# Kernel optimization log

Hardware: AMD Instinct MI355X
Metric: run time of the kernel (lower is better)

The kernel has to match this reference:

```python
import jax, jax.numpy as jnp
import numpy as np

B, S, D, H, DH, L, W, V, FF, HID = 2, 4096, 768, 12, 64, 12, 256, 50265, 3072, 384
SEL = np.arange(64) * 64  # index_select positions


def layer_norm(x, g, b):
    m = x.mean(-1, keepdims=True)
    v = ((x - m) ** 2).mean(-1, keepdims=True)
    return (x - m) * jax.lax.rsqrt(v + 1e-5) * g + b


def band_attention(q, k, v, key_mask):
    # q,k,v: [B,H,S,DH]; key_mask: [B,S] bool. Sliding window attention,
    # one-sided window W (total window 2W+1), via overlapping key chunks.
    nc = S // W
    qc = q.reshape(B, H, nc, W, DH)
    kp = jnp.pad(k, ((0, 0), (0, 0), (W, W), (0, 0)))
    vp = jnp.pad(v, ((0, 0), (0, 0), (W, W), (0, 0)))
    idx = jnp.arange(nc)[:, None] * W + jnp.arange(3 * W)[None, :]  # [nc,3W]
    kc = kp[:, :, idx]  # [B,H,nc,3W,DH]
    vc = vp[:, :, idx]
    scores = jnp.einsum('bhcid,bhcjd->bhcij', qc, kc) / np.float32(np.sqrt(DH))
    i = jnp.arange(W)[:, None]
    j = jnp.arange(3 * W)[None, :]
    band = (j >= i) & (j <= i + 2 * W)  # |key_pos - query_pos| <= W
    kmp = jnp.pad(key_mask, ((0, 0), (W, W)))
    kmc = kmp[:, idx]  # [B,nc,3W] key validity (in-range and non-pad)
    m = band[None, None, None] & kmc[:, None, :, None, :]
    scores = jnp.where(m, scores, -1e9)
    p = jax.nn.softmax(scores, axis=-1)
    ctx = jnp.einsum('bhcij,bhcjd->bhcid', p, vc)
    return ctx.reshape(B, H, S, DH)


def split_heads(x):
    return x.reshape(B, S, H, DH).transpose(0, 2, 1, 3)


def encoder(h, key_mask, layers):
    def step(h, p):
        Wq, bq, Wk, bk, Wv, bv, Wo, bo, g1, be1, W1, bf1, W2, bf2, g2, be2 = p
        q = split_heads(h @ Wq + bq)
        k = split_heads(h @ Wk + bk)
        v = split_heads(h @ Wv + bv)
        ctx = band_attention(q, k, v, key_mask).transpose(0, 2, 1, 3).reshape(B, S, D)
        h = layer_norm(h + ctx @ Wo + bo, g1, be1)
        ff = jax.nn.gelu(h @ W1 + bf1, approximate=False) @ W2 + bf2
        h = layer_norm(h + ff, g2, be2)
        return h, None
    h, _ = jax.lax.scan(jax.checkpoint(step), h, layers)
    return h


def lstm_scan(xs, Wi, Wh, b, reverse):
    # xs: [S,B,D]; torch gate order i,f,g,o
    def cell(carry, xt):
        h, c = carry
        g = xt @ Wi.T + h @ Wh.T + b
        gi, gf, gg, go = jnp.split(g, 4, axis=-1)
        c = jax.nn.sigmoid(gf) * c + jax.nn.sigmoid(gi) * jnp.tanh(gg)
        h = jax.nn.sigmoid(go) * jnp.tanh(c)
        return (h, c), h
    init = (jnp.zeros((B, HID), xs.dtype), jnp.zeros((B, HID), xs.dtype))
    _, hs = jax.lax.scan(cell, init, xs, reverse=reverse)
    return hs


def setup_inputs() -> dict:
    key = jax.random.key(0)
    ks = iter(jax.random.split(key, 40))
    std = 0.02
    n = lambda shape: jax.random.normal(next(ks), shape, jnp.float32) * std
    d = {
        'x': jax.random.randint(next(ks), (B, S), 0, V),
        'emb_w': n((V, D)), 'emb_p': n((S, D)),
        'ln_eg': jnp.ones((D,)), 'ln_eb': jnp.zeros((D,)),
        'Wq': n((L, D, D)), 'bq': jnp.zeros((L, D)),
        'Wk': n((L, D, D)), 'bk': jnp.zeros((L, D)),
        'Wv': n((L, D, D)), 'bv': jnp.zeros((L, D)),
        'Wo': n((L, D, D)), 'bo': jnp.zeros((L, D)),
        'ln1g': jnp.ones((L, D)), 'ln1b': jnp.zeros((L, D)),
        'W1': n((L, D, FF)), 'bf1': jnp.zeros((L, FF)),
        'W2': n((L, FF, D)), 'bf2': jnp.zeros((L, D)),
        'ln2g': jnp.ones((L, D)), 'ln2b': jnp.zeros((L, D)),
        'wi_f': n((4 * HID, D)), 'wh_f': n((4 * HID, HID)), 'b_f': jnp.zeros((4 * HID,)),
        'wi_b': n((4 * HID, D)), 'wh_b': n((4 * HID, HID)), 'b_b': jnp.zeros((4 * HID,)),
    }
    return d


def reference(x, emb_w, emb_p, ln_eg, ln_eb, Wq, bq, Wk, bk, Wv, bv, Wo, bo,
              ln1g, ln1b, W1, bf1, W2, bf2, ln2g, ln2b,
              wi_f, wh_f, b_f, wi_b, wh_b, b_b):
    key_mask = (x != 0)  # mask = (x != 0).float()
    h = layer_norm(emb_w[x] + emb_p[None, :S], ln_eg, ln_eb)
    layers = (Wq, bq, Wk, bk, Wv, bv, Wo, bo, ln1g, ln1b, W1, bf1, W2, bf2, ln2g, ln2b)
    h = encoder(h, key_mask, layers)
    xs = h.transpose(1, 0, 2)  # [S,B,D]
    hf = lstm_scan(xs, wi_f, wh_f, b_f, False)
    hb = lstm_scan(xs, wi_b, wh_b, b_b, True)
    rnn = jnp.concatenate([hf, hb], axis=-1).transpose(1, 0, 2)  # [B,S,D]
    return rnn[:, SEL]  # index_select -> [B,64,D]
```

## Files before the change

### kernel.cpp

```cpp
#include <hip/hip_runtime.h>


typedef short short8 __attribute__((ext_vector_type(8)));
typedef float float4_ __attribute__((ext_vector_type(4)));
typedef unsigned int uint2v __attribute__((ext_vector_type(2)));

#define GLOBAL_AS __attribute__((address_space(1)))
#define LDS_AS __attribute__((address_space(3)))

__device__ __forceinline__ short f2bf(float f) {
  union { float f; unsigned u; } x; x.f = f;
  unsigned r = (x.u + 0x7FFFu + ((x.u >> 16) & 1u)) >> 16;
  return (short)r;
}
__device__ __forceinline__ float sigm(float x) { return 1.0f / (1.0f + __expf(-x)); }
__device__ __forceinline__ float tanh_f(float x) { float e = __expf(2.0f * x); return 1.0f - 2.0f / (e + 1.0f); }

__device__ __forceinline__ void load_lds16(const void* g, void* l) {
  __builtin_amdgcn_global_load_lds((const GLOBAL_AS unsigned int*)g,
                                   (LDS_AS unsigned int*)l, 16, 0, 0);
}

__global__ void embed_kernel(const int* __restrict__ x, const float* __restrict__ emb_w,
                             const float* __restrict__ emb_p, float* __restrict__ tmp,
                             float* __restrict__ kmask) {
  int row = blockIdx.x;
  int s = row & 4095;
  int tok = x[row];
  const float* ew = emb_w + (size_t)tok * 768;
  const float* ep = emb_p + (size_t)s * 768;
  for (int i = threadIdx.x; i < 768; i += 256)
    tmp[(size_t)row * 768 + i] = ew[i] + ep[i];
  if (threadIdx.x == 0) kmask[row] = (tok != 0) ? 1.0f : 0.0f;
}

__global__ __launch_bounds__(256) void ln_kernel(const float* __restrict__ in,
    const float* __restrict__ g, const float* __restrict__ b,
    float* __restrict__ outf, short* __restrict__ outb, int rows) {
  int wave = threadIdx.x >> 6, lane = threadIdx.x & 63;
  int row = blockIdx.x * 4 + wave;
  if (row >= rows) return;
  const float* p = in + (size_t)row * 768;
  float v[12]; float s = 0.f, s2 = 0.f;
#pragma unroll
  for (int j = 0; j < 12; ++j) { v[j] = p[lane + j * 64]; s += v[j]; s2 += v[j] * v[j]; }
#pragma unroll
  for (int k = 1; k < 64; k <<= 1) { s += __shfl_xor(s, k); s2 += __shfl_xor(s2, k); }
  float mean = s * (1.0f / 768.0f);
  float var = s2 * (1.0f / 768.0f) - mean * mean;
  float rstd = rsqrtf(var + 1e-5f);
#pragma unroll
  for (int j = 0; j < 12; ++j) {
    int c = lane + j * 64;
    float o = (v[j] - mean) * rstd * g[c] + b[c];
    outf[(size_t)row * 768 + c] = o;
    outb[(size_t)row * 768 + c] = f2bf(o);
  }
}

__global__ __launch_bounds__(256) void prep_layer_kernel(
    const float* __restrict__ Wq, const float* __restrict__ Wk, const float* __restrict__ Wv,
    const float* __restrict__ Wo, const float* __restrict__ W1, const float* __restrict__ W2,
    const float* __restrict__ bq, const float* __restrict__ bk, const float* __restrict__ bv,
    short* __restrict__ wqkv, short* __restrict__ wo, short* __restrict__ w1,
    short* __restrict__ w2, float* __restrict__ biasqkv, int layer) {
  int bid = blockIdx.x;
  if (bid >= 6912) {
    int i = (bid - 6912) * 256 + threadIdx.x;
    if (i < 2304) {
      float v = (i < 768) ? bq[layer * 768 + i]
               : (i < 1536) ? bk[layer * 768 + i - 768] : bv[layer * 768 + i - 1536];
      biasqkv[i] = v;
    }
    return;
  }
  const float* src; short* dst; int R, C, tr, tc;
  if (bid < 1728) {
    int m = bid / 576; int tloc = bid % 576;
    src = (m == 0 ? Wq : (m == 1 ? Wk : Wv)) + (size_t)layer * 768 * 768;
    dst = wqkv + (size_t)m * 768 * 768; R = 768; C = 768; tr = tloc / 24; tc = tloc % 24;
  } else if (bid < 2304) {
    int tloc = bid - 1728; src = Wo + (size_t)layer * 768 * 768; dst = wo;
    R = 768; C = 768; tr = tloc / 24; tc = tloc % 24;
  } else if (bid < 4608) {
    int tloc = bid - 2304; src = W1 + (size_t)layer * 768 * 3072; dst = w1;
    R = 768; C = 3072; tr = tloc / 96; tc = tloc % 96;
  } else {
    int tloc = bid - 4608; src = W2 + (size_t)layer * 3072 * 768; dst = w2;
    R = 3072; C = 768; tr = tloc / 24; tc = tloc % 24;
  }
  __shared__ float tile[32][33];
  int tx = threadIdx.x & 31, ty = threadIdx.x >> 5;
#pragma unroll
  for (int i = 0; i < 4; ++i)
    tile[ty + i * 8][tx] = src[(size_t)(tr * 32 + ty + i * 8) * C + tc * 32 + tx];
  __syncthreads();
#pragma unroll
  for (int i = 0; i < 4; ++i) {
    int r = ty + i * 8;
    dst[(size_t)(tc * 32 + r) * R + tr * 32 + tx] = f2bf(tile[tx][r]);
  }
}

template <int MODE>
__global__ __launch_bounds__(256) void gemm_kernel(const short* __restrict__ A,
    const short* __restrict__ Bt, const float* __restrict__ bias,
    const float* __restrict__ res, float* __restrict__ outf, short* __restrict__ outb,
    int M, int N, int K, int ntn) {
  __shared__ short As[128 * 64];
  __shared__ short Bs[128 * 64];
  int tid = threadIdx.x;
  int wave = tid >> 6, lane = tid & 63;
  int l15 = lane & 15, qd = lane >> 4;
  int tm = blockIdx.x / ntn, tn = blockIdx.x % ntn;
  int wm = wave >> 1, wn = wave & 1;
  float4_ acc[4][4] = {};
  for (int k0 = 0; k0 < K; k0 += 64) {
    __syncthreads();
#pragma unroll
    for (int inst = 0; inst < 4; ++inst) {
      int i = inst * 256 + tid;
      const short* ga = A + (size_t)(tm * 128 + (i >> 3)) * K + k0 + (i & 7) * 8;
      const short* gb = Bt + (size_t)(tn * 128 + (i >> 3)) * K + k0 + (i & 7) * 8;
      int ldso = (inst * 256 + wave * 64) * 8;
      load_lds16(ga, &As[ldso]);
      load_lds16(gb, &Bs[ldso]);
    }
    __syncthreads();
#pragma unroll
    for (int ks = 0; ks < 2; ++ks) {
      short8 af[4], bf[4];
#pragma unroll
      for (int mt = 0; mt < 4; ++mt)
        af[mt] = *(const short8*)&As[(wm * 64 + mt * 16 + l15) * 64 + ks * 32 + qd * 8];
#pragma unroll
      for (int nt = 0; nt < 4; ++nt)
        bf[nt] = *(const short8*)&Bs[(wn * 64 + nt * 16 + l15) * 64 + ks * 32 + qd * 8];
#pragma unroll
      for (int mt = 0; mt < 4; ++mt)
#pragma unroll
        for (int nt = 0; nt < 4; ++nt)
          acc[mt][nt] = __builtin_amdgcn_mfma_f32_16x16x32_bf16(af[mt], bf[nt], acc[mt][nt], 0, 0, 0);
    }
  }
  int r0 = tm * 128 + wm * 64, c0 = tn * 128 + wn * 64;
#pragma unroll
  for (int nt = 0; nt < 4; ++nt) {
    int col = c0 + nt * 16 + l15;
    float bv = bias[col];
#pragma unroll
    for (int mt = 0; mt < 4; ++mt) {
      int rowb = r0 + mt * 16 + qd * 4;
#pragma unroll
      for (int r = 0; r < 4; ++r) {
        int row = rowb + r;
        float v = acc[mt][nt][r] + bv;
        if constexpr (MODE == 1) v = v * 0.5f * (1.0f + erff(v * 0.70710678f));
        if constexpr (MODE == 2) v += res[(size_t)row * N + col];
        if constexpr (MODE == 0 || MODE == 1) outb[(size_t)row * N + col] = f2bf(v);
        else outf[(size_t)row * N + col] = v;
      }
    }
  }
}

__global__ __launch_bounds__(256) void attn_kernel(const short* __restrict__ qkv,
    const float* __restrict__ kmask, short* __restrict__ ctx) {
  __shared__ short Ks[256 * 72];
  __shared__ short Vt[64 * 264];
  __shared__ float Ms[256];
  int bid = blockIdx.x;
  int qs = bid & 3; int c = (bid >> 2) & 15; int hh = bid >> 6;
  int head = hh % 12; int bt = hh / 12;
  int tid = threadIdx.x;
  int wave = tid >> 6, lane = tid & 63;
  int l15 = lane & 15, qd = lane >> 4;
  const float SCALE = 0.18033688f;

  short8 qf[2];
  {
    size_t srow = ((size_t)bt * 4096 + c * 256 + qs * 64 + wave * 16 + l15) * 2304;
#pragma unroll
    for (int ks = 0; ks < 2; ++ks)
      qf[ks] = *(const short8*)&qkv[srow + head * 64 + ks * 32 + qd * 8];
  }
  int iq = qs * 64 + wave * 16 + l15;

  float m_run = -1e9f, l_run = 0.0f;
  float4_ o4[4] = {};

  for (int kci = 0; kci < 3; ++kci) {
    int kc = c + kci - 1;
    if (kc < 0 || kc > 15) continue;
    __syncthreads();
    {
      int p = tid;
      size_t kr = ((size_t)bt * 4096 + kc * 256 + p) * 2304;
      int colv = (p & ~31) + (((p >> 2) & 3) << 3) + (((p >> 4) & 1) << 2) + (p & 3);
#pragma unroll
      for (int j8 = 0; j8 < 8; ++j8) {
        short8 kk = *(const short8*)&qkv[kr + 768 + head * 64 + j8 * 8];
        *(short8*)&Ks[p * 72 + j8 * 8] = kk;
        short8 vv = *(const short8*)&qkv[kr + 1536 + head * 64 + j8 * 8];
#pragma unroll
        for (int j = 0; j < 8; ++j) Vt[(j8 * 8 + j) * 264 + colv] = vv[j];
      }
      Ms[p] = kmask[bt * 4096 + kc * 256 + p];
    }
    __syncthreads();

    float4_ sc[16];
#pragma unroll
    for (int T = 0; T < 16; ++T) {
      float4_ a = {0.f, 0.f, 0.f, 0.f};
#pragma unroll
      for (int ks = 0; ks < 2; ++ks) {
        short8 kf = *(const short8*)&Ks[(T * 16 + l15) * 72 + ks * 32 + qd * 8];
        a = __builtin_amdgcn_mfma_f32_16x16x32_bf16(kf, qf[ks], a, 0, 0, 0);
      }
      sc[T] = a;
    }
    float cm = -1e9f;
#pragma unroll
    for (int T = 0; T < 16; ++T) {
      float4_ mk = *(const float4_*)&Ms[T * 16 + qd * 4];
#pragma unroll
      for (int r = 0; r < 4; ++r) {
        int key = T * 16 + qd * 4 + r;
        bool band = (kci == 1) || (kci == 0 ? (key >= iq) : (key <= iq));
        bool val = band && (mk[r] != 0.0f);
        float sv = val ? sc[T][r] * SCALE : -1e9f;
        sc[T][r] = sv;
        cm = fmaxf(cm, sv);
      }
    }
    cm = fmaxf(cm, __shfl_xor(cm, 16));
    cm = fmaxf(cm, __shfl_xor(cm, 32));
    float mnew = fmaxf(m_run, cm);
    float alpha = exp2f(m_run - mnew);
    m_run = mnew;
    l_run *= alpha;
#pragma unroll
    for (int mt = 0; mt < 4; ++mt) o4[mt] *= alpha;
#pragma unroll
    for (int T = 0; T < 16; ++T)
#pragma unroll
      for (int r = 0; r < 4; ++r) {
        float p = exp2f(sc[T][r] - mnew);
        sc[T][r] = p;
        l_run += p;
      }
#pragma unroll
    for (int ks = 0; ks < 8; ++ks) {
      short8 pb;
      pb[0] = f2bf(sc[2 * ks][0]);     pb[1] = f2bf(sc[2 * ks][1]);
      pb[2] = f2bf(sc[2 * ks][2]);     pb[3] = f2bf(sc[2 * ks][3]);
      pb[4] = f2bf(sc[2 * ks + 1][0]); pb[5] = f2bf(sc[2 * ks + 1][1]);
      pb[6] = f2bf(sc[2 * ks + 1][2]); pb[7] = f2bf(sc[2 * ks + 1][3]);
#pragma unroll
      for (int mt = 0; mt < 4; ++mt) {
        short8 va = *(const short8*)&Vt[(mt * 16 + l15) * 264 + ks * 32 + qd * 8];
        o4[mt] = __builtin_amdgcn_mfma_f32_16x16x32_bf16(va, pb, o4[mt], 0, 0, 0);
      }
    }
  }
  l_run += __shfl_xor(l_run, 16);
  l_run += __shfl_xor(l_run, 32);
  float rl = 1.0f / l_run;
  size_t crow = ((size_t)bt * 4096 + c * 256 + qs * 64 + wave * 16 + l15) * 768 + head * 64;
#pragma unroll
  for (int mt = 0; mt < 4; ++mt) {
    unsigned lo = (unsigned short)f2bf(o4[mt][0] * rl) |
                  ((unsigned)(unsigned short)f2bf(o4[mt][1] * rl) << 16);
    unsigned hi = (unsigned short)f2bf(o4[mt][2] * rl) |
                  ((unsigned)(unsigned short)f2bf(o4[mt][3] * rl) << 16);
    uint2v pk; pk[0] = lo; pk[1] = hi;
    *(uint2v*)&ctx[crow + mt * 16 + qd * 4] = pk;
  }
}

__global__ void lstm_prep_kernel(const float* __restrict__ wi_f, const float* __restrict__ wi_b,
    const float* __restrict__ wh_f, const float* __restrict__ wh_b,
    short* __restrict__ wi_bf, short* __restrict__ wh_bf) {
  size_t idx = (size_t)blockIdx.x * 256 + threadIdx.x;
  const size_t NWI = 1179648, NWH = 589824;
  if (idx < 2 * NWI) {
    const float* s = idx < NWI ? wi_f : wi_b;
    size_t k = idx < NWI ? idx : idx - NWI;
    wi_bf[idx] = f2bf(s[k]);
  } else {
    size_t k = idx - 2 * NWI;
    int d = k >= NWH;
    size_t kk = d ? k - NWH : k;
    int row = (int)(kk / 384), col = (int)(kk % 384);
    int w = row >> 7, g = (row >> 5) & 3, j = row & 31;
    const float* s = d ? wh_b : wh_f;
    wh_bf[k] = f2bf(s[(size_t)(g * 384 + w * 32 + j) * 384 + col]);
  }
}

__global__ void lstm_init_kernel(short* __restrict__ hbuf, unsigned* __restrict__ cnt) {
  int idx = blockIdx.x * 256 + threadIdx.x;
  if (idx < 24576) hbuf[idx] = 0;
  if (idx < 64) cnt[idx] = 0;
}

__global__ __launch_bounds__(256) void lstm_kernel(const short* __restrict__ Whb,
    const float* __restrict__ G, short* __restrict__ hbuf, unsigned* __restrict__ cnt,
    float* __restrict__ out) {
  int wg = blockIdx.x; int dir = wg / 12; int w = wg - dir * 12;
  int tid = threadIdx.x; int wave = tid >> 6; int lane = tid & 63;
  int l15 = lane & 15, qd = lane >> 4;
  __shared__ float gbuf[4][2][32];
  __shared__ float cst[64];
  short8 afrag[2][12];
#pragma unroll
  for (int tt = 0; tt < 2; ++tt)
#pragma unroll
    for (int ks = 0; ks < 12; ++ks)
      afrag[tt][ks] = *(const short8*)&Whb[((size_t)dir * 1536 + w * 128 + wave * 32 + tt * 16 + l15) * 384 + ks * 32 + qd * 8];
  if (tid < 64) cst[tid] = 0.0f;
  __syncthreads();
  unsigned* mycnt = cnt + dir * 16;
  for (int s = 0; s < 4096; ++s) {
    int t = dir ? (4095 - s) : s;
    if (s > 0) {
      if (tid == 0) {
        unsigned tgt = 12u * (unsigned)s;
        while (__hip_atomic_load(mycnt, __ATOMIC_ACQUIRE, __HIP_MEMORY_SCOPE_AGENT) < tgt)
          __builtin_amdgcn_s_sleep(1);
      }
      __syncthreads();
    }
    const short* hb = hbuf + (size_t)(dir * 2 + (s & 1)) * 16 * 384;
    short8 bfrag[12];
#pragma unroll
    for (int ks = 0; ks < 12; ++ks)
      bfrag[ks] = *(const short8*)&hb[l15 * 384 + ks * 32 + qd * 8];
    float gin[4] = {0.f, 0.f, 0.f, 0.f};
    if (tid < 64) {
      int j = tid & 31, bb = tid >> 5;
      const float* Gp = G + ((size_t)dir * 8192 + bb * 4096 + t) * 1536 + w * 32 + j;
#pragma unroll
      for (int g = 0; g < 4; ++g) gin[g] = Gp[g * 384];
    }
    float4_ acc0 = {0.f, 0.f, 0.f, 0.f}, acc1 = {0.f, 0.f, 0.f, 0.f};
#pragma unroll
    for (int ks = 0; ks < 12; ++ks) {
      acc0 = __builtin_amdgcn_mfma_f32_16x16x32_bf16(afrag[0][ks], bfrag[ks], acc0, 0, 0, 0);
      acc1 = __builtin_amdgcn_mfma_f32_16x16x32_bf16(afrag[1][ks], bfrag[ks], acc1, 0, 0, 0);
    }
    if (l15 < 2) {
#pragma unroll
      for (int r = 0; r < 4; ++r) {
        gbuf[wave][l15][qd * 4 + r] = acc0[r];
        gbuf[wave][l15][16 + qd * 4 + r] = acc1[r];
      }
    }
    __syncthreads();
    if (tid < 64) {
      int j = tid & 31, bb = tid >> 5;
      float gi = gbuf[0][bb][j] + gin[0];
      float gf = gbuf[1][bb][j] + gin[1];
      float gg = gbuf[2][bb][j] + gin[2];
      float go = gbuf[3][bb][j] + gin[3];
      float cc = sigm(gf) * cst[tid] + sigm(gi) * tanh_f(gg);
      cst[tid] = cc;
      float hh2 = sigm(go) * tanh_f(cc);
      hbuf[((size_t)(dir * 2 + ((s + 1) & 1)) * 16 + bb) * 384 + w * 32 + j] = f2bf(hh2);
      if ((t & 63) == 0)
        out[((size_t)bb * 64 + (t >> 6)) * 768 + dir * 384 + w * 32 + j] = hh2;
    }
    __threadfence();
    __syncthreads();
    if (tid == 0) atomicAdd(mycnt, 1u);
  }
}

extern "C" void kernel_launch(void* const* d_in, const int* in_sizes, int n_in,
                              void* d_out, int out_size, void* d_ws, size_t ws_size,
                              hipStream_t stream) {
  const int*   x     = (const int*)d_in[0];
  const float* emb_w = (const float*)d_in[1];
  const float* emb_p = (const float*)d_in[2];
  const float* ln_eg = (const float*)d_in[3];
  const float* ln_eb = (const float*)d_in[4];
  const float* Wq    = (const float*)d_in[5];
  const float* bq    = (const float*)d_in[6];
  const float* Wk    = (const float*)d_in[7];
  const float* bk    = (const float*)d_in[8];
  const float* Wv    = (const float*)d_in[9];
  const float* bv    = (const float*)d_in[10];
  const float* Wo    = (const float*)d_in[11];
  const float* bo    = (const float*)d_in[12];
  const float* ln1g  = (const float*)d_in[13];
  const float* ln1b  = (const float*)d_in[14];
  const float* W1    = (const float*)d_in[15];
  const float* bf1   = (const float*)d_in[16];
  const float* W2    = (const float*)d_in[17];
  const float* bf2   = (const float*)d_in[18];
  const float* ln2g  = (const float*)d_in[19];
  const float* ln2b  = (const float*)d_in[20];
  const float* wi_f  = (const float*)d_in[21];
  const float* wh_f  = (const float*)d_in[22];
  const float* b_f   = (const float*)d_in[23];
  const float* wi_b  = (const float*)d_in[24];
  const float* wh_b  = (const float*)d_in[25];
  const float* b_b   = (const float*)d_in[26];

  char* ws = (char*)d_ws;
  size_t off = 0;
  auto alloc = [&](size_t n) { size_t o = off; off += (n + 255) & ~(size_t)255; return o; };
  float* h_f32    = (float*)(ws + alloc(8192ull * 768 * 4));
  short* h_b16    = (short*)(ws + alloc(8192ull * 768 * 2));
  size_t alias0   = alloc(125829120ull);
  short* qkv      = (short*)(ws + alias0);
  short* ctx      = (short*)(ws + alias0 + 37748736ull);
  float* tmp      = (float*)(ws + alias0 + 50331648ull);
  short* ffn1     = (short*)(ws + alias0 + 75497472ull);
  float* G        = (float*)(ws + alias0);
  short* wqkv_t   = (short*)(ws + alloc(2304ull * 768 * 2));
  short* wo_t     = (short*)(ws + alloc(768ull * 768 * 2));
  short* w1_t     = (short*)(ws + alloc(3072ull * 768 * 2));
  short* w2_t     = (short*)(ws + alloc(768ull * 3072 * 2));
  float* biasqkv  = (float*)(ws + alloc(2304 * 4));
  short* wi_bf    = (short*)(ws + alloc(2ull * 1536 * 768 * 2));
  short* wh_bf    = (short*)(ws + alloc(2ull * 1536 * 384 * 2));
  short* hbuf     = (short*)(ws + alloc(2ull * 2 * 16 * 384 * 2));
  unsigned* cnt   = (unsigned*)(ws + alloc(256));
  float* kmask    = (float*)(ws + alloc(8192 * 4));
  if (ws_size < off) return;

  embed_kernel<<<8192, 256, 0, stream>>>(x, emb_w, emb_p, tmp, kmask);
  ln_kernel<<<2048, 256, 0, stream>>>(tmp, ln_eg, ln_eb, h_f32, h_b16, 8192);

  for (int l = 0; l < 12; ++l) {
    prep_layer_kernel<<<6921, 256, 0, stream>>>(Wq, Wk, Wv, Wo, W1, W2, bq, bk, bv,
                                                wqkv_t, wo_t, w1_t, w2_t, biasqkv, l);
    gemm_kernel<0><<<64 * 18, 256, 0, stream>>>(h_b16, wqkv_t, biasqkv, nullptr,
                                                nullptr, qkv, 8192, 2304, 768, 18);
    attn_kernel<<<1536, 256, 0, stream>>>(qkv, kmask, ctx);
    gemm_kernel<2><<<64 * 6, 256, 0, stream>>>(ctx, wo_t, bo + l * 768, h_f32,
                                               tmp, nullptr, 8192, 768, 768, 6);
    ln_kernel<<<2048, 256, 0, stream>>>(tmp, ln1g + l * 768, ln1b + l * 768, h_f32, h_b16, 8192);
    gemm_kernel<1><<<64 * 24, 256, 0, stream>>>(h_b16, w1_t, bf1 + l * 3072, nullptr,
                                                nullptr, ffn1, 8192, 3072, 768, 24);
    gemm_kernel<2><<<64 * 6, 256, 0, stream>>>(ffn1, w2_t, bf2 + l * 768, h_f32,
                                               tmp, nullptr, 8192, 768, 3072, 6);
    ln_kernel<<<2048, 256, 0, stream>>>(tmp, ln2g + l * 768, ln2b + l * 768, h_f32, h_b16, 8192);
  }

  lstm_prep_kernel<<<13824, 256, 0, stream>>>(wi_f, wi_b, wh_f, wh_b, wi_bf, wh_bf);
  gemm_kernel<3><<<64 * 12, 256, 0, stream>>>(h_b16, wi_bf, b_f, nullptr,
                                              G, nullptr, 8192, 1536, 768, 12);
  gemm_kernel<3><<<64 * 12, 256, 0, stream>>>(h_b16, wi_bf + 1536ull * 768, b_b, nullptr,
                                              G + 8192ull * 1536, nullptr, 8192, 1536, 768, 12);
  lstm_init_kernel<<<96, 256, 0, stream>>>(hbuf, cnt);
  lstm_kernel<<<24, 256, 0, stream>>>(wh_bf, G, hbuf, cnt, (float*)d_out);
}
```

Measured before the change: 23.43 ms.

## Restructure LSTM recurrence to 4 workgroups per direction with lighter cross-block sync

Each LSTM direction now runs on 4 workgroups instead of 12. Each workgroup keeps 96 hidden units of recurrent weights in registers (6 MFMA tiles per wave), and the prep kernel lays the weights out to match. Per-step synchronisation is lighter: relaxed atomics replace acquire loads and threadfences, the trailing block barrier is gone, only two batch rows of h are loaded, and the next step's input gates are prefetched. The aim is to cut the per-timestep cost of the global barrier across the 4096 sequential steps. In exchange each workgroup does three times the matrix work per step, and the relaxed memory ordering risks visibility bugs.

```diff
diff --git a/kernel.cpp b/kernel.cpp
--- a/kernel.cpp
+++ b/kernel.cpp
@@ -293,9 +293,10 @@
     int d = k >= NWH;
     size_t kk = d ? k - NWH : k;
     int row = (int)(kk / 384), col = (int)(kk % 384);
-    int w = row >> 7, g = (row >> 5) & 3, j = row & 31;
+    int w = row / 384, rem = row % 384;
+    int g = rem / 96, dd = rem % 96;
     const float* s = d ? wh_b : wh_f;
-    wh_bf[k] = f2bf(s[(size_t)(g * 384 + w * 32 + j) * 384 + col]);
+    wh_bf[k] = f2bf(s[(size_t)(g * 384 + w * 96 + dd) * 384 + col]);
   }
 }
 
@@ -305,75 +306,108 @@
   if (idx < 64) cnt[idx] = 0;
 }
 
-__global__ __launch_bounds__(256) void lstm_kernel(const short* __restrict__ Whb,
+__global__ __launch_bounds__(256, 1) void lstm_kernel(const short* __restrict__ Whb,
     const float* __restrict__ G, short* __restrict__ hbuf, unsigned* __restrict__ cnt,
     float* __restrict__ out) {
-  int wg = blockIdx.x; int dir = wg / 12; int w = wg - dir * 12;
+  int wg = blockIdx.x; int dir = wg >> 2; int w = wg & 3;
   int tid = threadIdx.x; int wave = tid >> 6; int lane = tid & 63;
   int l15 = lane & 15, qd = lane >> 4;
-  __shared__ float gbuf[4][2][32];
-  __shared__ float cst[64];
-  short8 afrag[2][12];
-#pragma unroll
-  for (int tt = 0; tt < 2; ++tt)
+  __shared__ float gbuf[4][2][96];
+
+  short8 afrag[6][12];
+#pragma unroll
+  for (int tt = 0; tt < 6; ++tt)
 #pragma unroll
     for (int ks = 0; ks < 12; ++ks)
-      afrag[tt][ks] = *(const short8*)&Whb[((size_t)dir * 1536 + w * 128 + wave * 32 + tt * 16 + l15) * 384 + ks * 32 + qd * 8];
-  if (tid < 64) cst[tid] = 0.0f;
-  __syncthreads();
+      afrag[tt][ks] = *(const short8*)&Whb[
+          ((size_t)dir * 1536 + w * 384 + wave * 96 + tt * 16 + l15) * 384 + ks * 32 + qd * 8];
+
   unsigned* mycnt = cnt + dir * 16;
+  int pj[3], pb[3];
+#pragma unroll
+  for (int k = 0; k < 3; ++k) { int p = lane + 64 * k; pb[k] = (p >= 96) ? 1 : 0; pj[k] = p - pb[k] * 96; }
+  float cst[3] = {0.f, 0.f, 0.f};
+  float ginC[3][4], ginN[3][4];
+  if (wave == 0) {
+    int t0 = dir ? 4095 : 0;
+#pragma unroll
+    for (int k = 0; k < 3; ++k) {
+      const float* Gp = G + ((size_t)dir * 8192 + pb[k] * 4096 + t0) * 1536 + w * 96 + pj[k];
+#pragma unroll
+      for (int g = 0; g < 4; ++g) ginC[k][g] = Gp[g * 384];
+    }
+  }
+
   for (int s = 0; s < 4096; ++s) {
     int t = dir ? (4095 - s) : s;
     if (s > 0) {
-      if (tid == 0) {
-        unsigned tgt = 12u * (unsigned)s;
-        while (__hip_atomic_load(mycnt, __ATOMIC_ACQUIRE, __HIP_MEMORY_SCOPE_AGENT) < tgt)
+      if (lane == 0) {
+        unsigned tgt = 4u * (unsigned)s;
+        while (__hip_atomic_load(mycnt, __ATOMIC_RELAXED, __HIP_MEMORY_SCOPE_AGENT) < tgt)
           __builtin_amdgcn_s_sleep(1);
       }
-      __syncthreads();
-    }
-    const short* hb = hbuf + (size_t)(dir * 2 + (s & 1)) * 16 * 384;
-    short8 bfrag[12];
+      asm volatile("" ::: "memory");
+    }
+    const short* hb = hbuf + (size_t)(dir * 2 + (s & 1)) * 2 * 384;
+    short8 bfrag[12] = {};
+    if (l15 < 2) {
+      const unsigned long long* hp = (const unsigned long long*)(hb + l15 * 384 + qd * 8);
+#pragma unroll
+      for (int ks = 0; ks < 12; ++ks) {
+        union { unsigned long long q[2]; short8 v; } u;
+        u.q[0] = __hip_atomic_load(hp + ks * 8, __ATOMIC_RELAXED, __HIP_MEMORY_SCOPE_AGENT);
+        u.q[1] = __hip_atomic_load(hp + ks * 8 + 1, __ATOMIC_RELAXED, __HIP_MEMORY_SCOPE_AGENT);
+        bfrag[ks] = u.v;
+      }
+    }
+    float4_ acc[6] = {};
 #pragma unroll
     for (int ks = 0; ks < 12; ++ks)
-      bfrag[ks] = *(const short8*)&hb[l15 * 384 + ks * 32 + qd * 8];
-    float gin[4] = {0.f, 0.f, 0.f, 0.f};
-    if (tid < 64) {
-      int j = tid & 31, bb = tid >> 5;
-      const float* Gp = G + ((size_t)dir * 8192 + bb * 4096 + t) * 1536 + w * 32 + j;
-#pragma unroll
-      for (int g = 0; g < 4; ++g) gin[g] = Gp[g * 384];
-    }
-    float4_ acc0 = {0.f, 0.f, 0.f, 0.f}, acc1 = {0.f, 0.f, 0.f, 0.f};
-#pragma unroll
-    for (int ks = 0; ks < 12; ++ks) {
-      acc0 = __builtin_amdgcn_mfma_f32_16x16x32_bf16(afrag[0][ks], bfrag[ks], acc0, 0, 0, 0);
-      acc1 = __builtin_amdgcn_mfma_f32_16x16x32_bf16(afrag[1][ks], bfrag[ks], acc1, 0, 0, 0);
-    }
+#pragma unroll
+      for (int tt = 0; tt < 6; ++tt)
+        acc[tt] = __builtin_amdgcn_mfma_f32_16x16x32_bf16(afrag[tt][ks], bfrag[ks], acc[tt], 0, 0, 0);
     if (l15 < 2) {
 #pragma unroll
-      for (int r = 0; r < 4; ++r) {
-        gbuf[wave][l15][qd * 4 + r] = acc0[r];
-        gbuf[wave][l15][16 + qd * 4 + r] = acc1[r];
-      }
+      for (int tt = 0; tt < 6; ++tt)
+        *(float4_*)&gbuf[wave][l15][tt * 16 + qd * 4] = acc[tt];
     }
     __syncthreads();
-    if (tid < 64) {
-      int j = tid & 31, bb = tid >> 5;
-      float gi = gbuf[0][bb][j] + gin[0];
-      float gf = gbuf[1][bb][j] + gin[1];
-      float gg = gbuf[2][bb][j] + gin[2];
-      float go = gbuf[3][bb][j] + gin[3];
-      float cc = sigm(gf) * cst[tid] + sigm(gi) * tanh_f(gg);
-      cst[tid] = cc;
-      float hh2 = sigm(go) * tanh_f(cc);
-      hbuf[((size_t)(dir * 2 + ((s + 1) & 1)) * 16 + bb) * 384 + w * 32 + j] = f2bf(hh2);
-      if ((t & 63) == 0)
-        out[((size_t)bb * 64 + (t >> 6)) * 768 + dir * 384 + w * 32 + j] = hh2;
-    }
-    __threadfence();
-    __syncthreads();
-    if (tid == 0) atomicAdd(mycnt, 1u);
+    if (wave == 0) {
+      if (s > 0) {
+#pragma unroll
+        for (int k = 0; k < 3; ++k)
+#pragma unroll
+          for (int g = 0; g < 4; ++g) ginC[k][g] = ginN[k][g];
+      }
+      short* hn = hbuf + (size_t)(dir * 2 + ((s + 1) & 1)) * 2 * 384;
+#pragma unroll
+      for (int k = 0; k < 3; ++k) {
+        int j = pj[k], bb = pb[k];
+        float gi = gbuf[0][bb][j] + ginC[k][0];
+        float gf = gbuf[1][bb][j] + ginC[k][1];
+        float gg = gbuf[2][bb][j] + ginC[k][2];
+        float go = gbuf[3][bb][j] + ginC[k][3];
+        float cc = sigm(gf) * cst[k] + sigm(gi) * tanh_f(gg);
+        cst[k] = cc;
+        float hh2 = sigm(go) * tanh_f(cc);
+        __hip_atomic_store(&hn[bb * 384 + w * 96 + j], f2bf(hh2),
+                           __ATOMIC_RELAXED, __HIP_MEMORY_SCOPE_AGENT);
+        if ((t & 63) == 0)
+          out[((size_t)bb * 64 + (t >> 6)) * 768 + dir * 384 + w * 96 + j] = hh2;
+      }
+      asm volatile("s_waitcnt vmcnt(0)" ::: "memory");
+      if (lane == 0)
+        __hip_atomic_fetch_add(mycnt, 1u, __ATOMIC_RELAXED, __HIP_MEMORY_SCOPE_AGENT);
+      if (s + 1 < 4096) {
+        int t2 = dir ? (4095 - (s + 1)) : (s + 1);
+#pragma unroll
+        for (int k = 0; k < 3; ++k) {
+          const float* Gp = G + ((size_t)dir * 8192 + pb[k] * 4096 + t2) * 1536 + w * 96 + pj[k];
+#pragma unroll
+          for (int g = 0; g < 4; ++g) ginN[k][g] = Gp[g * 384];
+        }
+      }
+    }
   }
 }
 
@@ -456,5 +490,5 @@
   gemm_kernel<3><<<64 * 12, 256, 0, stream>>>(h_b16, wi_bf + 1536ull * 768, b_b, nullptr,
                                               G + 8192ull * 1536, nullptr, 8192, 1536, 768, 12);
   lstm_init_kernel<<<96, 256, 0, stream>>>(hbuf, cnt);
-  lstm_kernel<<<24, 256, 0, stream>>>(wh_bf, G, hbuf, cnt, (float*)d_out);
-}
+  lstm_kernel<<<8, 256, 0, stream>>>(wh_bf, G, hbuf, cnt, (float*)d_out);
+}
```

Measured after the change: 20.37 ms. 1.15x faster.
